# Optimization experiments

Hardware: AMD Instinct MI355X
Metric: run time of the kernel (lower is better)

Reference implementation:

```python
import jax, jax.numpy as jnp
import numpy as np

N_NODES = 50000
N_EDGES = 800000
D_IN = 64
D_OUT = 64


def setup_inputs() -> dict:
    key = jax.random.key(0)
    k1, k2, k3, k4, k5 = jax.random.split(key, 5)
    feat = jax.random.normal(k1, (N_NODES, D_IN), dtype=jnp.float32)
    # torch Linear layout: W [out_feats, in_feats]
    W = jax.random.normal(k2, (D_OUT, D_IN), dtype=jnp.float32) * (1.0 / np.sqrt(D_IN))
    b = jax.random.normal(k3, (D_OUT,), dtype=jnp.float32) * 0.01
    eps = jnp.zeros((1,), dtype=jnp.float32)
    src = jax.random.randint(k4, (N_EDGES,), 0, N_NODES, dtype=jnp.int32)
    dst = jax.random.randint(k5, (N_EDGES,), 0, N_NODES, dtype=jnp.int32)
    return {"feat": feat, "W": W, "b": b, "eps": eps, "src": src, "dst": dst}


def reference(feat, W, b, eps, src, dst):
    # message = feat[src]; sum-aggregate per destination node
    neigh = jax.ops.segment_sum(feat[src], dst, num_segments=N_NODES)  # [N, D_in]
    rst = (1.0 + eps) * feat + neigh                                   # eps-scaled residual
    out = rst @ W.T + b                                                # Linear (torch layout)
    return out
```

## Files before the change

kernel.cpp:

```cpp
#include <hip/hip_runtime.h>

constexpr int N_NODES = 50000;
constexpr int N_EDGES = 800000;
constexpr int D = 64;

constexpr int NREG = 256;
constexpr int RSZ = 196;
constexpr int EPB = 4096;
constexpr int NBINB = 196;
constexpr int CELLCAP = 64;
constexpr int RECAP = 4608;

constexpr int WS_CNT2 = 0;
constexpr int WS_RBUF = 50176;
constexpr size_t WS_HB_BYTE = (size_t)(50176 + (size_t)NREG * NBINB * CELLCAP) * 4;

using vfloat4 = __attribute__((ext_vector_type(4))) float;

__device__ __forceinline__ ushort to_bf16(float x) {
  unsigned u = __float_as_uint(x);
  u += 0x7FFF + ((u >> 16) & 1);
  return (ushort)(u >> 16);
}
__device__ __forceinline__ float from_bf16(ushort h) {
  return __uint_as_float((unsigned)h << 16);
}

__global__ __launch_bounds__(1024) void prep_kernel(
    const float4* __restrict__ feat4, const int* __restrict__ src,
    const int* __restrict__ dst, ushort* __restrict__ hb,
    int* __restrict__ cnt2, unsigned* __restrict__ rbuf) {
  __shared__ int cur[NREG];
  int tid = threadIdx.x, blk = blockIdx.x;
  if (tid < NREG) cur[tid] = 0;

  int e0 = blk * EPB + tid * 4;
  bool valid = (e0 + 4 <= N_EDGES);
  int4 d4 = {0, 0, 0, 0}, s4 = {0, 0, 0, 0};
  if (valid) {
    d4 = *reinterpret_cast<const int4*>(dst + e0);
    s4 = *reinterpret_cast<const int4*>(src + e0);
  }

  int cb = blk * 4096 + tid;
#pragma unroll
  for (int k = 0; k < 4; ++k) {
    int t = cb + k * 1024;
    if (t < N_NODES * D / 4) {
      float4 f = feat4[t];
      ushort4 h;
      h.x = to_bf16(f.x); h.y = to_bf16(f.y);
      h.z = to_bf16(f.z); h.w = to_bf16(f.w);
      *reinterpret_cast<ushort4*>(hb + t * 4) = h;
    }
  }
  __syncthreads();

  if (valid) {
    const int dd[4] = {d4.x, d4.y, d4.z, d4.w};
    const int ss[4] = {s4.x, s4.y, s4.z, s4.w};
#pragma unroll
    for (int k = 0; k < 4; ++k) {
      int r = dd[k] / RSZ;
      unsigned pk = ((unsigned)(dd[k] - r * RSZ) << 16) | (unsigned)ss[k];
      int p = atomicAdd(&cur[r], 1);
      if (p < CELLCAP)
        rbuf[(size_t)(r * NBINB + blk) * CELLCAP + p] = pk;
    }
  }
  __syncthreads();
  if (tid < NREG) {
    int c = cur[tid];
    cnt2[tid * NBINB + blk] = (c > CELLCAP) ? CELLCAP : c;
  }
}

__global__ __launch_bounds__(1024) void gin_kernel(
    const float* __restrict__ feat, const ushort* __restrict__ hb,
    const float* __restrict__ W, const float* __restrict__ b,
    const float* __restrict__ eps, const int* __restrict__ cnt2,
    const unsigned* __restrict__ rbuf, float* __restrict__ out) {
  __shared__ float Wt[D * D];
  __shared__ unsigned ebuf[RECAP];
  __shared__ ushort sorted[RECAP];
  __shared__ int cellstart[NBINB + 1];
  __shared__ int hist[RSZ], nstart[RSZ + 1], cursor[RSZ];
  __shared__ int scan_tmp[256];

  int tid = threadIdx.x, r = blockIdx.x;
  for (int q = tid; q < D * D; q += 1024) Wt[q] = W[((q & 63) << 6) + (q >> 6)];
  if (tid < RSZ) hist[tid] = 0;

  int c = (tid < NBINB) ? cnt2[r * NBINB + tid] : 0;
  if (tid < 256) scan_tmp[tid] = c;
  __syncthreads();
  for (int ofs = 1; ofs < 256; ofs <<= 1) {
    int v = 0;
    if (tid < 256 && tid >= ofs) v = scan_tmp[tid - ofs];
    __syncthreads();
    if (tid < 256) scan_tmp[tid] += v;
    __syncthreads();
  }
  if (tid < NBINB) cellstart[tid] = scan_tmp[tid] - c;
  if (tid == NBINB - 1) cellstart[NBINB] = scan_tmp[tid];
  __syncthreads();
  int T = cellstart[NBINB];
  if (T > RECAP) T = RECAP;

  {
    int blk2 = tid >> 2, sub = tid & 3;
    if (blk2 < NBINB) {
      int cs = cellstart[blk2];
      int cc = cellstart[blk2 + 1] - cs;
      const unsigned* cell = rbuf + (size_t)(r * NBINB + blk2) * CELLCAP;
      for (int i = sub * 4; i < cc; i += 16) {
        uint4 v = *reinterpret_cast<const uint4*>(cell + i);
        if (cs + i + 0 < T && i + 0 < cc) ebuf[cs + i + 0] = v.x;
        if (cs + i + 1 < T && i + 1 < cc) ebuf[cs + i + 1] = v.y;
        if (cs + i + 2 < T && i + 2 < cc) ebuf[cs + i + 2] = v.z;
        if (cs + i + 3 < T && i + 3 < cc) ebuf[cs + i + 3] = v.w;
      }
    }
  }
  __syncthreads();

  for (int e = tid; e < T; e += 1024) atomicAdd(&hist[ebuf[e] >> 16], 1);
  __syncthreads();
  if (tid < 256) scan_tmp[tid] = (tid < RSZ) ? hist[tid] : 0;
  __syncthreads();
  for (int ofs = 1; ofs < 256; ofs <<= 1) {
    int v = 0;
    if (tid < 256 && tid >= ofs) v = scan_tmp[tid - ofs];
    __syncthreads();
    if (tid < 256) scan_tmp[tid] += v;
    __syncthreads();
  }
  if (tid < RSZ) {
    int ex = scan_tmp[tid] - hist[tid];
    nstart[tid] = ex;
    cursor[tid] = ex;
  }
  if (tid == RSZ - 1) nstart[RSZ] = scan_tmp[tid];
  __syncthreads();
  for (int e = tid; e < T; e += 1024) {
    unsigned pk = ebuf[e];
    int p = atomicAdd(&cursor[pk >> 16], 1);
    sorted[p] = (ushort)(pk & 0xFFFFu);
  }
  __syncthreads();

  int g = tid >> 4, j4 = (tid & 15) << 2;
  float s = 1.0f + eps[0];

  for (int n = g; n < RSZ; n += 64) {
    int node = r * RSZ + n;
    if (node >= N_NODES) continue;

    vfloat4 fin = __builtin_nontemporal_load(
        reinterpret_cast<const vfloat4*>(feat + (node << 6) + j4));
    float4 acc;
    acc.x = fin.x * s; acc.y = fin.y * s; acc.z = fin.z * s; acc.w = fin.w * s;

    int e = nstart[n], e1 = nstart[n + 1];
    for (; e + 8 <= e1; e += 8) {
      int i0 = sorted[e + 0], i1 = sorted[e + 1], i2 = sorted[e + 2], i3 = sorted[e + 3];
      int i4_ = sorted[e + 4], i5 = sorted[e + 5], i6 = sorted[e + 6], i7 = sorted[e + 7];
      ushort4 h0 = *reinterpret_cast<const ushort4*>(hb + (i0 << 6) + j4);
      ushort4 h1 = *reinterpret_cast<const ushort4*>(hb + (i1 << 6) + j4);
      ushort4 h2 = *reinterpret_cast<const ushort4*>(hb + (i2 << 6) + j4);
      ushort4 h3 = *reinterpret_cast<const ushort4*>(hb + (i3 << 6) + j4);
      ushort4 h4 = *reinterpret_cast<const ushort4*>(hb + (i4_ << 6) + j4);
      ushort4 h5 = *reinterpret_cast<const ushort4*>(hb + (i5 << 6) + j4);
      ushort4 h6 = *reinterpret_cast<const ushort4*>(hb + (i6 << 6) + j4);
      ushort4 h7 = *reinterpret_cast<const ushort4*>(hb + (i7 << 6) + j4);
      acc.x += (from_bf16(h0.x) + from_bf16(h1.x)) + (from_bf16(h2.x) + from_bf16(h3.x))
             + (from_bf16(h4.x) + from_bf16(h5.x)) + (from_bf16(h6.x) + from_bf16(h7.x));
      acc.y += (from_bf16(h0.y) + from_bf16(h1.y)) + (from_bf16(h2.y) + from_bf16(h3.y))
             + (from_bf16(h4.y) + from_bf16(h5.y)) + (from_bf16(h6.y) + from_bf16(h7.y));
      acc.z += (from_bf16(h0.z) + from_bf16(h1.z)) + (from_bf16(h2.z) + from_bf16(h3.z))
             + (from_bf16(h4.z) + from_bf16(h5.z)) + (from_bf16(h6.z) + from_bf16(h7.z));
      acc.w += (from_bf16(h0.w) + from_bf16(h1.w)) + (from_bf16(h2.w) + from_bf16(h3.w))
             + (from_bf16(h4.w) + from_bf16(h5.w)) + (from_bf16(h6.w) + from_bf16(h7.w));
    }
    for (; e < e1; ++e) {
      int sn = sorted[e];
      ushort4 h = *reinterpret_cast<const ushort4*>(hb + (sn << 6) + j4);
      acc.x += from_bf16(h.x); acc.y += from_bf16(h.y);
      acc.z += from_bf16(h.z); acc.w += from_bf16(h.w);
    }

    float4 res = *reinterpret_cast<const float4*>(b + j4);
#pragma unroll
    for (int i4 = 0; i4 < 16; ++i4) {
      float rx = __shfl(acc.x, i4, 16);
      float ry = __shfl(acc.y, i4, 16);
      float rz = __shfl(acc.z, i4, 16);
      float rw = __shfl(acc.w, i4, 16);
      const float4 w0 = *reinterpret_cast<const float4*>(Wt + ((i4 << 2) + 0) * D + j4);
      const float4 w1 = *reinterpret_cast<const float4*>(Wt + ((i4 << 2) + 1) * D + j4);
      const float4 w2 = *reinterpret_cast<const float4*>(Wt + ((i4 << 2) + 2) * D + j4);
      const float4 w3 = *reinterpret_cast<const float4*>(Wt + ((i4 << 2) + 3) * D + j4);
      res.x += rx * w0.x + ry * w1.x + rz * w2.x + rw * w3.x;
      res.y += rx * w0.y + ry * w1.y + rz * w2.y + rw * w3.y;
      res.z += rx * w0.z + ry * w1.z + rz * w2.z + rw * w3.z;
      res.w += rx * w0.w + ry * w1.w + rz * w2.w + rw * w3.w;
    }
    vfloat4 vres;
    vres.x = res.x; vres.y = res.y; vres.z = res.z; vres.w = res.w;
    __builtin_nontemporal_store(
        vres, reinterpret_cast<vfloat4*>(out + (node << 6) + j4));
  }
}

extern "C" void kernel_launch(void* const* d_in, const int* in_sizes, int n_in,
                              void* d_out, int out_size, void* d_ws, size_t ws_size,
                              hipStream_t stream) {
  const float* feat = (const float*)d_in[0];
  const float* W    = (const float*)d_in[1];
  const float* b    = (const float*)d_in[2];
  const float* eps  = (const float*)d_in[3];
  const int*   src  = (const int*)d_in[4];
  const int*   dst  = (const int*)d_in[5];
  float* out = (float*)d_out;

  int* ws = (int*)d_ws;
  int* cnt2      = ws + WS_CNT2;
  unsigned* rbuf = (unsigned*)(ws + WS_RBUF);
  ushort* hb     = (ushort*)((char*)d_ws + WS_HB_BYTE);

  hipLaunchKernelGGL(prep_kernel, dim3(NBINB), dim3(1024), 0, stream,
                     (const float4*)feat, src, dst, hb, cnt2, rbuf);
  hipLaunchKernelGGL(gin_kernel, dim3(NREG), dim3(1024), 0, stream,
                     feat, hb, W, b, eps, cnt2, rbuf, out);
}
```

Before: 112.8 us.

## Fuse prep and aggregation into one cooperative kernel, drop bf16 feature copy

Merges the edge-binning prep kernel and the aggregation/linear kernel into a single cooperative launch with a grid-wide sync between phases, removing a kernel launch boundary. It also drops the bf16 copy of the features and gathers fp32 rows directly, trading the conversion pass for twice the bytes per gathered row. The edge binning is re-partitioned to 256 blocks of 3125 edges with a smaller cell capacity of 48. Nontemporal loads and stores are replaced by ordinary ones. Risks include cooperative launch overhead and losing edges if a cell exceeds 48 entries.

After: 159.0 us. +41.0%, slower.

```diff
diff --git a/kernel.cpp b/kernel.cpp
--- a/kernel.cpp
+++ b/kernel.cpp
@@ -1,97 +1,62 @@
 #include <hip/hip_runtime.h>
+#include <hip/hip_cooperative_groups.h>
+
+namespace cg = cooperative_groups;
 
 constexpr int N_NODES = 50000;
 constexpr int N_EDGES = 800000;
 constexpr int D = 64;
 
-constexpr int NREG = 256;
+constexpr int NBLK = 256;
 constexpr int RSZ = 196;
-constexpr int EPB = 4096;
-constexpr int NBINB = 196;
-constexpr int CELLCAP = 64;
+constexpr int EPB = 3125;
+constexpr int CELLCAP = 48;
 constexpr int RECAP = 4608;
 
 constexpr int WS_CNT2 = 0;
-constexpr int WS_RBUF = 50176;
-constexpr size_t WS_HB_BYTE = (size_t)(50176 + (size_t)NREG * NBINB * CELLCAP) * 4;
+constexpr int WS_RBUF = NBLK * NBLK;
 
-using vfloat4 = __attribute__((ext_vector_type(4))) float;
-
-__device__ __forceinline__ ushort to_bf16(float x) {
-  unsigned u = __float_as_uint(x);
-  u += 0x7FFF + ((u >> 16) & 1);
-  return (ushort)(u >> 16);
-}
-__device__ __forceinline__ float from_bf16(ushort h) {
-  return __uint_as_float((unsigned)h << 16);
-}
-
-__global__ __launch_bounds__(1024) void prep_kernel(
-    const float4* __restrict__ feat4, const int* __restrict__ src,
-    const int* __restrict__ dst, ushort* __restrict__ hb,
-    int* __restrict__ cnt2, unsigned* __restrict__ rbuf) {
-  __shared__ int cur[NREG];
-  int tid = threadIdx.x, blk = blockIdx.x;
-  if (tid < NREG) cur[tid] = 0;
-
-  int e0 = blk * EPB + tid * 4;
-  bool valid = (e0 + 4 <= N_EDGES);
-  int4 d4 = {0, 0, 0, 0}, s4 = {0, 0, 0, 0};
-  if (valid) {
-    d4 = *reinterpret_cast<const int4*>(dst + e0);
-    s4 = *reinterpret_cast<const int4*>(src + e0);
-  }
-
-  int cb = blk * 4096 + tid;
-#pragma unroll
-  for (int k = 0; k < 4; ++k) {
-    int t = cb + k * 1024;
-    if (t < N_NODES * D / 4) {
-      float4 f = feat4[t];
-      ushort4 h;
-      h.x = to_bf16(f.x); h.y = to_bf16(f.y);
-      h.z = to_bf16(f.z); h.w = to_bf16(f.w);
-      *reinterpret_cast<ushort4*>(hb + t * 4) = h;
-    }
-  }
-  __syncthreads();
-
-  if (valid) {
-    const int dd[4] = {d4.x, d4.y, d4.z, d4.w};
-    const int ss[4] = {s4.x, s4.y, s4.z, s4.w};
-#pragma unroll
-    for (int k = 0; k < 4; ++k) {
-      int r = dd[k] / RSZ;
-      unsigned pk = ((unsigned)(dd[k] - r * RSZ) << 16) | (unsigned)ss[k];
-      int p = atomicAdd(&cur[r], 1);
-      if (p < CELLCAP)
-        rbuf[(size_t)(r * NBINB + blk) * CELLCAP + p] = pk;
-    }
-  }
-  __syncthreads();
-  if (tid < NREG) {
-    int c = cur[tid];
-    cnt2[tid * NBINB + blk] = (c > CELLCAP) ? CELLCAP : c;
-  }
-}
-
-__global__ __launch_bounds__(1024) void gin_kernel(
-    const float* __restrict__ feat, const ushort* __restrict__ hb,
-    const float* __restrict__ W, const float* __restrict__ b,
-    const float* __restrict__ eps, const int* __restrict__ cnt2,
-    const unsigned* __restrict__ rbuf, float* __restrict__ out) {
+__global__ __launch_bounds__(1024) void gin_coop_kernel(
+    const float* __restrict__ feat, const float* __restrict__ W,
+    const float* __restrict__ b, const float* __restrict__ eps,
+    const int* __restrict__ src, const int* __restrict__ dst,
+    int* __restrict__ cnt2, unsigned* __restrict__ rbuf,
+    float* __restrict__ out) {
   __shared__ float Wt[D * D];
   __shared__ unsigned ebuf[RECAP];
   __shared__ ushort sorted[RECAP];
-  __shared__ int cellstart[NBINB + 1];
+  __shared__ int cellstart[NBLK + 1];
   __shared__ int hist[RSZ], nstart[RSZ + 1], cursor[RSZ];
   __shared__ int scan_tmp[256];
+  __shared__ int cur[NBLK];
 
-  int tid = threadIdx.x, r = blockIdx.x;
+  cg::grid_group grid = cg::this_grid();
+  int tid = threadIdx.x, blk = blockIdx.x;
+
+  if (tid < NBLK) cur[tid] = 0;
+  __syncthreads();
+  int e0 = blk * EPB;
+  for (int i = tid; i < EPB; i += 1024) {
+    int d = dst[e0 + i];
+    int s = src[e0 + i];
+    int r = d / RSZ;
+    unsigned pk = ((unsigned)(d - r * RSZ) << 16) | (unsigned)s;
+    int p = atomicAdd(&cur[r], 1);
+    if (p < CELLCAP) rbuf[(r * NBLK + blk) * CELLCAP + p] = pk;
+  }
   for (int q = tid; q < D * D; q += 1024) Wt[q] = W[((q & 63) << 6) + (q >> 6)];
+  __syncthreads();
+  if (tid < NBLK) {
+    int c = cur[tid];
+    cnt2[tid * NBLK + blk] = (c > CELLCAP) ? CELLCAP : c;
+  }
+
+  grid.sync();
+
+  int r = blk;
   if (tid < RSZ) hist[tid] = 0;
 
-  int c = (tid < NBINB) ? cnt2[r * NBINB + tid] : 0;
+  int c = (tid < NBLK) ? cnt2[r * NBLK + tid] : 0;
   if (tid < 256) scan_tmp[tid] = c;
   __syncthreads();
   for (int ofs = 1; ofs < 256; ofs <<= 1) {
@@ -101,25 +66,23 @@
     if (tid < 256) scan_tmp[tid] += v;
     __syncthreads();
   }
-  if (tid < NBINB) cellstart[tid] = scan_tmp[tid] - c;
-  if (tid == NBINB - 1) cellstart[NBINB] = scan_tmp[tid];
+  if (tid < NBLK) cellstart[tid] = scan_tmp[tid] - c;
+  if (tid == NBLK - 1) cellstart[NBLK] = scan_tmp[tid];
   __syncthreads();
-  int T = cellstart[NBINB];
+  int T = cellstart[NBLK];
   if (T > RECAP) T = RECAP;
 
   {
-    int blk2 = tid >> 2, sub = tid & 3;
-    if (blk2 < NBINB) {
-      int cs = cellstart[blk2];
-      int cc = cellstart[blk2 + 1] - cs;
-      const unsigned* cell = rbuf + (size_t)(r * NBINB + blk2) * CELLCAP;
-      for (int i = sub * 4; i < cc; i += 16) {
-        uint4 v = *reinterpret_cast<const uint4*>(cell + i);
-        if (cs + i + 0 < T && i + 0 < cc) ebuf[cs + i + 0] = v.x;
-        if (cs + i + 1 < T && i + 1 < cc) ebuf[cs + i + 1] = v.y;
-        if (cs + i + 2 < T && i + 2 < cc) ebuf[cs + i + 2] = v.z;
-        if (cs + i + 3 < T && i + 3 < cc) ebuf[cs + i + 3] = v.w;
-      }
+    int cell = tid >> 2, sub = tid & 3;
+    int cs = cellstart[cell];
+    int cc = cellstart[cell + 1] - cs;
+    const unsigned* cp = rbuf + (size_t)(r * NBLK + cell) * CELLCAP;
+    for (int i = sub * 4; i < cc; i += 16) {
+      uint4 v = *reinterpret_cast<const uint4*>(cp + i);
+      if (cs + i + 0 < T && i + 0 < cc) ebuf[cs + i + 0] = v.x;
+      if (cs + i + 1 < T && i + 1 < cc) ebuf[cs + i + 1] = v.y;
+      if (cs + i + 2 < T && i + 2 < cc) ebuf[cs + i + 2] = v.z;
+      if (cs + i + 3 < T && i + 3 < cc) ebuf[cs + i + 3] = v.w;
     }
   }
   __syncthreads();
@@ -156,37 +119,30 @@
     int node = r * RSZ + n;
     if (node >= N_NODES) continue;
 
-    vfloat4 fin = __builtin_nontemporal_load(
-        reinterpret_cast<const vfloat4*>(feat + (node << 6) + j4));
-    float4 acc;
-    acc.x = fin.x * s; acc.y = fin.y * s; acc.z = fin.z * s; acc.w = fin.w * s;
+    float4 acc = *reinterpret_cast<const float4*>(feat + (node << 6) + j4);
+    acc.x *= s; acc.y *= s; acc.z *= s; acc.w *= s;
 
     int e = nstart[n], e1 = nstart[n + 1];
     for (; e + 8 <= e1; e += 8) {
       int i0 = sorted[e + 0], i1 = sorted[e + 1], i2 = sorted[e + 2], i3 = sorted[e + 3];
       int i4_ = sorted[e + 4], i5 = sorted[e + 5], i6 = sorted[e + 6], i7 = sorted[e + 7];
-      ushort4 h0 = *reinterpret_cast<const ushort4*>(hb + (i0 << 6) + j4);
-      ushort4 h1 = *reinterpret_cast<const ushort4*>(hb + (i1 << 6) + j4);
-      ushort4 h2 = *reinterpret_cast<const ushort4*>(hb + (i2 << 6) + j4);
-      ushort4 h3 = *reinterpret_cast<const ushort4*>(hb + (i3 << 6) + j4);
-      ushort4 h4 = *reinterpret_cast<const ushort4*>(hb + (i4_ << 6) + j4);
-      ushort4 h5 = *reinterpret_cast<const ushort4*>(hb + (i5 << 6) + j4);
-      ushort4 h6 = *reinterpret_cast<const ushort4*>(hb + (i6 << 6) + j4);
-      ushort4 h7 = *reinterpret_cast<const ushort4*>(hb + (i7 << 6) + j4);
-      acc.x += (from_bf16(h0.x) + from_bf16(h1.x)) + (from_bf16(h2.x) + from_bf16(h3.x))
-             + (from_bf16(h4.x) + from_bf16(h5.x)) + (from_bf16(h6.x) + from_bf16(h7.x));
-      acc.y += (from_bf16(h0.y) + from_bf16(h1.y)) + (from_bf16(h2.y) + from_bf16(h3.y))
-             + (from_bf16(h4.y) + from_bf16(h5.y)) + (from_bf16(h6.y) + from_bf16(h7.y));
-      acc.z += (from_bf16(h0.z) + from_bf16(h1.z)) + (from_bf16(h2.z) + from_bf16(h3.z))
-             + (from_bf16(h4.z) + from_bf16(h5.z)) + (from_bf16(h6.z) + from_bf16(h7.z));
-      acc.w += (from_bf16(h0.w) + from_bf16(h1.w)) + (from_bf16(h2.w) + from_bf16(h3.w))
-             + (from_bf16(h4.w) + from_bf16(h5.w)) + (from_bf16(h6.w) + from_bf16(h7.w));
+      const float4 f0 = *reinterpret_cast<const float4*>(feat + (i0 << 6) + j4);
+      const float4 f1 = *reinterpret_cast<const float4*>(feat + (i1 << 6) + j4);
+      const float4 f2 = *reinterpret_cast<const float4*>(feat + (i2 << 6) + j4);
+      const float4 f3 = *reinterpret_cast<const float4*>(feat + (i3 << 6) + j4);
+      const float4 f4 = *reinterpret_cast<const float4*>(feat + (i4_ << 6) + j4);
+      const float4 f5 = *reinterpret_cast<const float4*>(feat + (i5 << 6) + j4);
+      const float4 f6 = *reinterpret_cast<const float4*>(feat + (i6 << 6) + j4);
+      const float4 f7 = *reinterpret_cast<const float4*>(feat + (i7 << 6) + j4);
+      acc.x += (f0.x + f1.x) + (f2.x + f3.x) + (f4.x + f5.x) + (f6.x + f7.x);
+      acc.y += (f0.y + f1.y) + (f2.y + f3.y) + (f4.y + f5.y) + (f6.y + f7.y);
+      acc.z += (f0.z + f1.z) + (f2.z + f3.z) + (f4.z + f5.z) + (f6.z + f7.z);
+      acc.w += (f0.w + f1.w) + (f2.w + f3.w) + (f4.w + f5.w) + (f6.w + f7.w);
     }
     for (; e < e1; ++e) {
       int sn = sorted[e];
-      ushort4 h = *reinterpret_cast<const ushort4*>(hb + (sn << 6) + j4);
-      acc.x += from_bf16(h.x); acc.y += from_bf16(h.y);
-      acc.z += from_bf16(h.z); acc.w += from_bf16(h.w);
+      const float4 f = *reinterpret_cast<const float4*>(feat + (sn << 6) + j4);
+      acc.x += f.x; acc.y += f.y; acc.z += f.z; acc.w += f.w;
     }
 
     float4 res = *reinterpret_cast<const float4*>(b + j4);
@@ -205,10 +161,7 @@
       res.z += rx * w0.z + ry * w1.z + rz * w2.z + rw * w3.z;
       res.w += rx * w0.w + ry * w1.w + rz * w2.w + rw * w3.w;
     }
-    vfloat4 vres;
-    vres.x = res.x; vres.y = res.y; vres.z = res.z; vres.w = res.w;
-    __builtin_nontemporal_store(
-        vres, reinterpret_cast<vfloat4*>(out + (node << 6) + j4));
+    *reinterpret_cast<float4*>(out + (node << 6) + j4) = res;
   }
 }
 
@@ -226,10 +179,10 @@
   int* ws = (int*)d_ws;
   int* cnt2      = ws + WS_CNT2;
   unsigned* rbuf = (unsigned*)(ws + WS_RBUF);
-  ushort* hb     = (ushort*)((char*)d_ws + WS_HB_BYTE);
 
-  hipLaunchKernelGGL(prep_kernel, dim3(NBINB), dim3(1024), 0, stream,
-                     (const float4*)feat, src, dst, hb, cnt2, rbuf);
-  hipLaunchKernelGGL(gin_kernel, dim3(NREG), dim3(1024), 0, stream,
-                     feat, hb, W, b, eps, cnt2, rbuf, out);
+  void* args[] = {(void*)&feat, (void*)&W, (void*)&b, (void*)&eps,
+                  (void*)&src, (void*)&dst, (void*)&cnt2, (void*)&rbuf,
+                  (void*)&out};
+  hipLaunchCooperativeKernel((const void*)gin_coop_kernel, dim3(NBLK),
+                             dim3(1024), args, 0, stream);
 }
```

## Process two nodes per 8-lane group with 16-byte bf16 gathers and shared W reads

Applied to the files above, without the earlier changes.

The gather phase now assigns 8 lanes per node, with each lane holding 8 features. Neighbor rows are fetched as 16-byte uint4 loads instead of 8-byte ushort4. Each group handles two nodes, n and n+128, and runs a fused matvec in which each W row read from shared memory feeds both nodes' outputs. This halves LDS weight traffic per node and widens memory transactions, but raises register pressure at 1024 threads per block and serialises the two nodes' gathers inside one thread.

Result: slower. 338.6 us (+200.2%).

```diff
diff --git a/kernel.cpp b/kernel.cpp
--- a/kernel.cpp
+++ b/kernel.cpp
@@ -22,8 +22,11 @@
   u += 0x7FFF + ((u >> 16) & 1);
   return (ushort)(u >> 16);
 }
-__device__ __forceinline__ float from_bf16(ushort h) {
-  return __uint_as_float((unsigned)h << 16);
+__device__ __forceinline__ float bf_lo(unsigned u) {
+  return __uint_as_float(u << 16);
+}
+__device__ __forceinline__ float bf_hi(unsigned u) {
+  return __uint_as_float(u & 0xFFFF0000u);
 }
 
 __global__ __launch_bounds__(1024) void prep_kernel(
@@ -108,13 +111,13 @@
   if (T > RECAP) T = RECAP;
 
   {
-    int blk2 = tid >> 2, sub = tid & 3;
-    if (blk2 < NBINB) {
-      int cs = cellstart[blk2];
-      int cc = cellstart[blk2 + 1] - cs;
-      const unsigned* cell = rbuf + (size_t)(r * NBINB + blk2) * CELLCAP;
+    int cell = tid >> 2, sub = tid & 3;
+    if (cell < NBINB) {
+      int cs = cellstart[cell];
+      int cc = cellstart[cell + 1] - cs;
+      const unsigned* cp = rbuf + (size_t)(r * NBINB + cell) * CELLCAP;
       for (int i = sub * 4; i < cc; i += 16) {
-        uint4 v = *reinterpret_cast<const uint4*>(cell + i);
+        uint4 v = *reinterpret_cast<const uint4*>(cp + i);
         if (cs + i + 0 < T && i + 0 < cc) ebuf[cs + i + 0] = v.x;
         if (cs + i + 1 < T && i + 1 < cc) ebuf[cs + i + 1] = v.y;
         if (cs + i + 2 < T && i + 2 < cc) ebuf[cs + i + 2] = v.z;
@@ -149,66 +152,97 @@
   }
   __syncthreads();
 
-  int g = tid >> 4, j4 = (tid & 15) << 2;
+  int g = tid >> 3, j8 = (tid & 7) << 3;
   float s = 1.0f + eps[0];
 
-  for (int n = g; n < RSZ; n += 64) {
-    int node = r * RSZ + n;
-    if (node >= N_NODES) continue;
-
-    vfloat4 fin = __builtin_nontemporal_load(
-        reinterpret_cast<const vfloat4*>(feat + (node << 6) + j4));
-    float4 acc;
-    acc.x = fin.x * s; acc.y = fin.y * s; acc.z = fin.z * s; acc.w = fin.w * s;
-
+  int n0 = g, n1 = g + 128;
+  int node0 = r * RSZ + n0, node1 = r * RSZ + n1;
+  bool valid0 = (n0 < RSZ) && (node0 < N_NODES);
+  bool valid1 = (n1 < RSZ) && (node1 < N_NODES);
+
+  float acc0[8] = {0, 0, 0, 0, 0, 0, 0, 0};
+  float acc1[8] = {0, 0, 0, 0, 0, 0, 0, 0};
+
+#pragma unroll
+  for (int which = 0; which < 2; ++which) {
+    bool valid = which ? valid1 : valid0;
+    if (!valid) continue;
+    int n = which ? n1 : n0;
+    int node = which ? node1 : node0;
+    float* acc = which ? acc1 : acc0;
+
+    {
+      const float4 fa = *reinterpret_cast<const float4*>(feat + (node << 6) + j8);
+      const float4 fb = *reinterpret_cast<const float4*>(feat + (node << 6) + j8 + 4);
+      acc[0] = s * fa.x; acc[1] = s * fa.y; acc[2] = s * fa.z; acc[3] = s * fa.w;
+      acc[4] = s * fb.x; acc[5] = s * fb.y; acc[6] = s * fb.z; acc[7] = s * fb.w;
+    }
     int e = nstart[n], e1 = nstart[n + 1];
     for (; e + 8 <= e1; e += 8) {
-      int i0 = sorted[e + 0], i1 = sorted[e + 1], i2 = sorted[e + 2], i3 = sorted[e + 3];
-      int i4_ = sorted[e + 4], i5 = sorted[e + 5], i6 = sorted[e + 6], i7 = sorted[e + 7];
-      ushort4 h0 = *reinterpret_cast<const ushort4*>(hb + (i0 << 6) + j4);
-      ushort4 h1 = *reinterpret_cast<const ushort4*>(hb + (i1 << 6) + j4);
-      ushort4 h2 = *reinterpret_cast<const ushort4*>(hb + (i2 << 6) + j4);
-      ushort4 h3 = *reinterpret_cast<const ushort4*>(hb + (i3 << 6) + j4);
-      ushort4 h4 = *reinterpret_cast<const ushort4*>(hb + (i4_ << 6) + j4);
-      ushort4 h5 = *reinterpret_cast<const ushort4*>(hb + (i5 << 6) + j4);
-      ushort4 h6 = *reinterpret_cast<const ushort4*>(hb + (i6 << 6) + j4);
-      ushort4 h7 = *reinterpret_cast<const ushort4*>(hb + (i7 << 6) + j4);
-      acc.x += (from_bf16(h0.x) + from_bf16(h1.x)) + (from_bf16(h2.x) + from_bf16(h3.x))
-             + (from_bf16(h4.x) + from_bf16(h5.x)) + (from_bf16(h6.x) + from_bf16(h7.x));
-      acc.y += (from_bf16(h0.y) + from_bf16(h1.y)) + (from_bf16(h2.y) + from_bf16(h3.y))
-             + (from_bf16(h4.y) + from_bf16(h5.y)) + (from_bf16(h6.y) + from_bf16(h7.y));
-      acc.z += (from_bf16(h0.z) + from_bf16(h1.z)) + (from_bf16(h2.z) + from_bf16(h3.z))
-             + (from_bf16(h4.z) + from_bf16(h5.z)) + (from_bf16(h6.z) + from_bf16(h7.z));
-      acc.w += (from_bf16(h0.w) + from_bf16(h1.w)) + (from_bf16(h2.w) + from_bf16(h3.w))
-             + (from_bf16(h4.w) + from_bf16(h5.w)) + (from_bf16(h6.w) + from_bf16(h7.w));
+      uint4 h[8];
+#pragma unroll
+      for (int k = 0; k < 8; ++k) {
+        int sn = sorted[e + k];
+        h[k] = *reinterpret_cast<const uint4*>(hb + (sn << 6) + j8);
+      }
+#pragma unroll
+      for (int k = 0; k < 8; ++k) {
+        acc[0] += bf_lo(h[k].x); acc[1] += bf_hi(h[k].x);
+        acc[2] += bf_lo(h[k].y); acc[3] += bf_hi(h[k].y);
+        acc[4] += bf_lo(h[k].z); acc[5] += bf_hi(h[k].z);
+        acc[6] += bf_lo(h[k].w); acc[7] += bf_hi(h[k].w);
+      }
     }
     for (; e < e1; ++e) {
       int sn = sorted[e];
-      ushort4 h = *reinterpret_cast<const ushort4*>(hb + (sn << 6) + j4);
-      acc.x += from_bf16(h.x); acc.y += from_bf16(h.y);
-      acc.z += from_bf16(h.z); acc.w += from_bf16(h.w);
-    }
-
-    float4 res = *reinterpret_cast<const float4*>(b + j4);
-#pragma unroll
-    for (int i4 = 0; i4 < 16; ++i4) {
-      float rx = __shfl(acc.x, i4, 16);
-      float ry = __shfl(acc.y, i4, 16);
-      float rz = __shfl(acc.z, i4, 16);
-      float rw = __shfl(acc.w, i4, 16);
-      const float4 w0 = *reinterpret_cast<const float4*>(Wt + ((i4 << 2) + 0) * D + j4);
-      const float4 w1 = *reinterpret_cast<const float4*>(Wt + ((i4 << 2) + 1) * D + j4);
-      const float4 w2 = *reinterpret_cast<const float4*>(Wt + ((i4 << 2) + 2) * D + j4);
-      const float4 w3 = *reinterpret_cast<const float4*>(Wt + ((i4 << 2) + 3) * D + j4);
-      res.x += rx * w0.x + ry * w1.x + rz * w2.x + rw * w3.x;
-      res.y += rx * w0.y + ry * w1.y + rz * w2.y + rw * w3.y;
-      res.z += rx * w0.z + ry * w1.z + rz * w2.z + rw * w3.z;
-      res.w += rx * w0.w + ry * w1.w + rz * w2.w + rw * w3.w;
-    }
-    vfloat4 vres;
-    vres.x = res.x; vres.y = res.y; vres.z = res.z; vres.w = res.w;
-    __builtin_nontemporal_store(
-        vres, reinterpret_cast<vfloat4*>(out + (node << 6) + j4));
+      uint4 hv = *reinterpret_cast<const uint4*>(hb + (sn << 6) + j8);
+      acc[0] += bf_lo(hv.x); acc[1] += bf_hi(hv.x);
+      acc[2] += bf_lo(hv.y); acc[3] += bf_hi(hv.y);
+      acc[4] += bf_lo(hv.z); acc[5] += bf_hi(hv.z);
+      acc[6] += bf_lo(hv.w); acc[7] += bf_hi(hv.w);
+    }
+  }
+
+  if (valid0) {
+    float res0[8], res1[8];
+    {
+      const float4 ba = *reinterpret_cast<const float4*>(b + j8);
+      const float4 bb = *reinterpret_cast<const float4*>(b + j8 + 4);
+      res0[0] = ba.x; res0[1] = ba.y; res0[2] = ba.z; res0[3] = ba.w;
+      res0[4] = bb.x; res0[5] = bb.y; res0[6] = bb.z; res0[7] = bb.w;
+#pragma unroll
+      for (int k = 0; k < 8; ++k) res1[k] = res0[k];
+    }
+#pragma unroll
+    for (int i = 0; i < D; ++i) {
+      int srcl = i >> 3, k = i & 7;
+      float r0 = __shfl(acc0[k], srcl, 8);
+      float r1 = __shfl(acc1[k], srcl, 8);
+      const float4 wa = *reinterpret_cast<const float4*>(Wt + i * D + j8);
+      const float4 wb = *reinterpret_cast<const float4*>(Wt + i * D + j8 + 4);
+      res0[0] += r0 * wa.x; res0[1] += r0 * wa.y;
+      res0[2] += r0 * wa.z; res0[3] += r0 * wa.w;
+      res0[4] += r0 * wb.x; res0[5] += r0 * wb.y;
+      res0[6] += r0 * wb.z; res0[7] += r0 * wb.w;
+      res1[0] += r1 * wa.x; res1[1] += r1 * wa.y;
+      res1[2] += r1 * wa.z; res1[3] += r1 * wa.w;
+      res1[4] += r1 * wb.x; res1[5] += r1 * wb.y;
+      res1[6] += r1 * wb.z; res1[7] += r1 * wb.w;
+    }
+    {
+      vfloat4 v;
+      v.x = res0[0]; v.y = res0[1]; v.z = res0[2]; v.w = res0[3];
+      __builtin_nontemporal_store(v, reinterpret_cast<vfloat4*>(out + (node0 << 6) + j8));
+      v.x = res0[4]; v.y = res0[5]; v.z = res0[6]; v.w = res0[7];
+      __builtin_nontemporal_store(v, reinterpret_cast<vfloat4*>(out + (node0 << 6) + j8 + 4));
+    }
+    if (valid1) {
+      vfloat4 v;
+      v.x = res1[0]; v.y = res1[1]; v.z = res1[2]; v.w = res1[3];
+      __builtin_nontemporal_store(v, reinterpret_cast<vfloat4*>(out + (node1 << 6) + j8));
+      v.x = res1[4]; v.y = res1[5]; v.z = res1[6]; v.w = res1[7];
+      __builtin_nontemporal_store(v, reinterpret_cast<vfloat4*>(out + (node1 << 6) + j8 + 4));
+    }
   }
 }
 
```
